# Optimization experiments

Hardware: AMD Instinct MI355X
Metric: run time of the kernel (lower is better)

The kernel has to match this reference:

```python
import jax, jax.numpy as jnp
import numpy as np

B, H, E = 1024, 2048, 1024

def _xavier(key, shape):
    # torch xavier_normal_ on [1, out, in]: std = sqrt(2/(fan_in+fan_out)) over last two dims
    fan_out, fan_in = shape[-2], shape[-1]
    std = (2.0 / (fan_in + fan_out)) ** 0.5
    return jax.random.normal(key, shape, jnp.float32) * std

def setup_inputs() -> dict:
    key = jax.random.key(0)
    ks = jax.random.split(key, 17)
    inp = {
        'x': jax.random.normal(ks[0], (B, E, 1), jnp.float32),
        'c': jax.random.normal(ks[1], (B, H, 1), jnp.float32),
        'h': jax.random.normal(ks[2], (B, H, 1), jnp.float32),
        'W_xi': _xavier(ks[3], (1, H, E)), 'W_hi': _xavier(ks[4], (1, H, H)), 'B_i': _xavier(ks[5], (1, H, 1)),
        'W_xg': _xavier(ks[6], (1, H, E)), 'W_hg': _xavier(ks[7], (1, H, H)), 'B_g': _xavier(ks[8], (1, H, 1)),
        'W_xf': _xavier(ks[9], (1, H, E)), 'W_hf': _xavier(ks[10], (1, H, H)), 'B_f': _xavier(ks[11], (1, H, 1)),
        'W_xo': _xavier(ks[12], (1, H, E)), 'W_ho': _xavier(ks[13], (1, H, H)), 'B_o': _xavier(ks[14], (1, H, 1)),
        'W_hy': _xavier(ks[15], (1, E, H)), 'B_y': _xavier(ks[16], (1, E, 1)),
    }
    return inp

def reference(x, c, h, W_xi, W_hi, B_i, W_xg, W_hg, B_g, W_xf, W_hf, B_f, W_xo, W_ho, B_o, W_hy, B_y):
    # jnp.matmul broadcasts the leading batch dim: [1,H,E] @ [B,E,1] -> [B,H,1]
    i = jax.nn.sigmoid(jnp.matmul(W_xi, x) + jnp.matmul(W_hi, h) + B_i)
    g = jnp.tanh(jnp.matmul(W_xg, x) + jnp.matmul(W_hg, h) + B_g)
    f = jax.nn.sigmoid(jnp.matmul(W_xf, x) + jnp.matmul(W_hf, h) + B_f)
    c_new = f * c + i * g
    o = jax.nn.sigmoid(jnp.matmul(W_xo, x) + jnp.matmul(W_ho, h) + B_o)
    h_new = o * c_new  # NOTE: source uses o*c (no tanh), faithful to original
    y = jnp.tanh(jnp.matmul(W_hy, h_new) + B_y)
    return (y, c_new, h_new)
```

## Files before the change

kernel.cpp:

```cpp
#include <hip/hip_runtime.h>

#define B_SZ 1024
#define H_SZ 2048
#define E_SZ 1024

typedef float  f32x4 __attribute__((ext_vector_type(4)));
typedef short  s16x8 __attribute__((ext_vector_type(8)));

__device__ __forceinline__ unsigned short f2bf(float f) {
    unsigned u = __float_as_uint(f);
    u = u + 0x7fffu + ((u >> 16) & 1u);
    return (unsigned short)(u >> 16);
}
__device__ __forceinline__ float bf2f(unsigned short s) {
    return __uint_as_float(((unsigned)s) << 16);
}
__device__ __forceinline__ float sigm(float v) {
    return 1.0f / (1.0f + __expf(-v));
}

struct SwArgs {
    const float*    src[11];
    unsigned short* dst[11];
    int             log2K[11];
    int             nthr[11];
};

__global__ __launch_bounds__(256) void swcast_kernel(SwArgs a) {
    const int arr = blockIdx.y;
    const int t = blockIdx.x * 256 + threadIdx.x;
    if (t >= a.nthr[arr]) return;
    const int lg   = a.log2K[arr];
    const int lane = t & 63;
    const int u    = t >> 6;
    const int hj   = u & 7;
    const int v    = u >> 3;
    const int k32m = (1 << (lg - 5)) - 1;
    const int ks   = v & k32m;
    const int nt   = v >> (lg - 5);
    const int row  = (nt << 7) + ((hj >> 2) << 6) + ((hj & 3) << 4) + (lane & 15);
    const int k    = (ks << 5) + ((lane >> 4) << 3);
    const float* s = a.src[arr] + ((size_t)row << lg) + k;
    float4 v0 = *(const float4*)s;
    float4 v1 = *(const float4*)(s + 4);
    s16x8 o;
    o[0] = (short)f2bf(v0.x); o[1] = (short)f2bf(v0.y);
    o[2] = (short)f2bf(v0.z); o[3] = (short)f2bf(v0.w);
    o[4] = (short)f2bf(v1.x); o[5] = (short)f2bf(v1.y);
    o[6] = (short)f2bf(v1.z); o[7] = (short)f2bf(v1.w);
    *(s16x8*)(a.dst[arr] + (size_t)t * 8) = o;
}

#define LDF(dst, base, ks)                                                  \
    _Pragma("unroll") for (int _i = 0; _i < 4; ++_i)                        \
        dst[_i] = *(const s16x8*)((base) + (ks) * 4096 + _i * 512);

#define MF(aa, bb)                                                          \
    _Pragma("unroll") for (int _i = 0; _i < 4; ++_i)                        \
    _Pragma("unroll") for (int _j = 0; _j < 4; ++_j)                        \
        acc[_i][_j] = __builtin_amdgcn_mfma_f32_16x16x32_bf16(              \
            aa[_i], bb[_j], acc[_i][_j], 0, 0, 0);

__global__ __launch_bounds__(256) void gates_kernel(
    const unsigned short* __restrict__ Xsw,
    const unsigned short* __restrict__ Hsw,
    const unsigned short* __restrict__ Wxsw,
    const unsigned short* __restrict__ Whsw,
    const float* __restrict__ bi, const float* __restrict__ bg,
    const float* __restrict__ bff, const float* __restrict__ bo,
    unsigned short* __restrict__ Z)
{
    const int t   = threadIdx.x;
    const int b   = blockIdx.x;
    const int xcd = b & 7;
    const int i_  = b >> 3;
    const int nt  = xcd * 8 + (i_ >> 3);
    const int mt  = i_ & 7;
    const int q   = nt >> 4;
    const int n0t = nt & 15;
    const int lane = t & 63, w = t >> 6;
    const int hm = w >> 1, hn = w & 1;

    const unsigned short* ax = Xsw + (size_t)(mt * 256 + hm * 4) * 512 + lane * 8;
    const unsigned short* bx = Wxsw + (size_t)q * H_SZ * E_SZ
                             + (size_t)(n0t * 256 + hn * 4) * 512 + lane * 8;
    const unsigned short* ah = Hsw + (size_t)(mt * 512 + hm * 4) * 512 + lane * 8;
    const unsigned short* bh = Whsw + (size_t)q * H_SZ * H_SZ
                             + (size_t)(n0t * 512 + hn * 4) * 512 + lane * 8;

    f32x4 acc[4][4] = {};
    s16x8 a0[4], b0[4], a1[4], b1[4];

    LDF(a0, ax, 0); LDF(b0, bx, 0);
    for (int ks = 0; ks < 30; ks += 2) {
        LDF(a1, ax, ks + 1); LDF(b1, bx, ks + 1);
        MF(a0, b0);
        LDF(a0, ax, ks + 2); LDF(b0, bx, ks + 2);
        MF(a1, b1);
    }
    LDF(a1, ax, 31); LDF(b1, bx, 31);
    MF(a0, b0);
    LDF(a0, ah, 0); LDF(b0, bh, 0);
    MF(a1, b1);
    for (int ks = 0; ks < 62; ks += 2) {
        LDF(a1, ah, ks + 1); LDF(b1, bh, ks + 1);
        MF(a0, b0);
        LDF(a0, ah, ks + 2); LDF(b0, bh, ks + 2);
        MF(a1, b1);
    }
    LDF(a1, ah, 63); LDF(b1, bh, 63);
    MF(a0, b0);
    MF(a1, b1);

    const float* bias = (q == 0) ? bi : (q == 1) ? bg : (q == 2) ? bff : bo;
    const int m0 = mt * 128, n0 = n0t * 128;
    const int wr = hm << 6, wc = hn << 6;
    const int lr = lane & 15, rq = (lane >> 4) << 2;
    unsigned short* Zq = Z + (size_t)q * B_SZ * H_SZ;
#pragma unroll
    for (int i = 0; i < 4; ++i) {
#pragma unroll
        for (int j = 0; j < 4; ++j) {
            const int n = n0 + wc + j * 16 + lr;
            const float bv = bias[n];
#pragma unroll
            for (int r = 0; r < 4; ++r) {
                const int m = m0 + wr + i * 16 + rq + r;
                const float v = acc[i][j][r] + bv;
                const float a = (q == 1) ? tanhf(v) : sigm(v);
                Zq[(size_t)m * H_SZ + n] = f2bf(a);
            }
        }
    }
}

__global__ __launch_bounds__(256) void cell_kernel(
    const unsigned short* __restrict__ Z, const float* __restrict__ c,
    float* __restrict__ c_out, float* __restrict__ h_out,
    unsigned short* __restrict__ Hnsw)
{
    const size_t BH = (size_t)B_SZ * H_SZ;
    const int t8 = blockIdx.x * 256 + threadIdx.x;
    const size_t base = (size_t)t8 * 8;

    s16x8 iu = *(const s16x8*)(Z + base);
    s16x8 gu = *(const s16x8*)(Z + BH + base);
    s16x8 fu = *(const s16x8*)(Z + 2 * BH + base);
    s16x8 ou = *(const s16x8*)(Z + 3 * BH + base);
    float4 c0 = *(const float4*)(c + base);
    float4 c1 = *(const float4*)(c + base + 4);
    const float cv[8] = {c0.x, c0.y, c0.z, c0.w, c1.x, c1.y, c1.z, c1.w};

    float cn[8], hn[8];
#pragma unroll
    for (int e = 0; e < 8; ++e) {
        cn[e] = bf2f((unsigned short)fu[e]) * cv[e]
              + bf2f((unsigned short)iu[e]) * bf2f((unsigned short)gu[e]);
        hn[e] = bf2f((unsigned short)ou[e]) * cn[e];
    }
    *(float4*)(c_out + base)     = make_float4(cn[0], cn[1], cn[2], cn[3]);
    *(float4*)(c_out + base + 4) = make_float4(cn[4], cn[5], cn[6], cn[7]);
    *(float4*)(h_out + base)     = make_float4(hn[0], hn[1], hn[2], hn[3]);
    *(float4*)(h_out + base + 4) = make_float4(hn[4], hn[5], hn[6], hn[7]);

    const int m  = (int)(base >> 11);
    const int hk = (int)(base & 2047);
    const int mt = m >> 7, half = (m >> 6) & 1, ii = (m >> 4) & 3, lr = m & 15;
    const int ks = hk >> 5, kq3 = (hk >> 3) & 3;
    const int lane2 = (kq3 << 4) | lr;
    const size_t toff = ((((size_t)mt * 64 + ks) * 8 + half * 4 + ii) * 64 + lane2) * 8;
    s16x8 hb;
#pragma unroll
    for (int e = 0; e < 8; ++e) hb[e] = (short)f2bf(hn[e]);
    *(s16x8*)(Hnsw + toff) = hb;
}

__global__ __launch_bounds__(256) void y_split_kernel(
    const unsigned short* __restrict__ Hnsw,
    const unsigned short* __restrict__ Whysw,
    float* __restrict__ part)
{
    const int t   = threadIdx.x;
    const int b   = blockIdx.x;
    const int xcd = b & 7;
    const int i_  = b >> 3;
    const int ns  = xcd * 4 + (i_ >> 3);
    const int mt  = i_ & 7;
    const int n0t = ns >> 2;
    const int s   = ns & 3;
    const int lane = t & 63, w = t >> 6;
    const int hm = w >> 1, hn = w & 1;

    const unsigned short* ay = Hnsw
        + (size_t)((mt * 64 + s * 16) * 8 + hm * 4) * 512 + lane * 8;
    const unsigned short* by = Whysw
        + (size_t)((n0t * 64 + s * 16) * 8 + hn * 4) * 512 + lane * 8;

    f32x4 acc[4][4] = {};
    s16x8 a0[4], b0[4], a1[4], b1[4];
    LDF(a0, ay, 0); LDF(b0, by, 0);
    for (int ks = 0; ks < 14; ks += 2) {
        LDF(a1, ay, ks + 1); LDF(b1, by, ks + 1);
        MF(a0, b0);
        LDF(a0, ay, ks + 2); LDF(b0, by, ks + 2);
        MF(a1, b1);
    }
    LDF(a1, ay, 15); LDF(b1, by, 15);
    MF(a0, b0);
    MF(a1, b1);

    const int m0 = mt * 128, n0 = n0t * 128;
    const int wr = hm << 6, wc = hn << 6;
    const int lr = lane & 15, rq = (lane >> 4) << 2;
    float* P = part + (size_t)s * B_SZ * E_SZ;
#pragma unroll
    for (int i = 0; i < 4; ++i) {
#pragma unroll
        for (int j = 0; j < 4; ++j) {
            const int n = n0 + wc + j * 16 + lr;
#pragma unroll
            for (int r = 0; r < 4; ++r) {
                const int m = m0 + wr + i * 16 + rq + r;
                P[(size_t)m * E_SZ + n] = acc[i][j][r];
            }
        }
    }
}

__global__ __launch_bounds__(256) void y_reduce_kernel(
    const float* __restrict__ part, const float* __restrict__ by,
    float* __restrict__ yout)
{
    const size_t BE = (size_t)B_SZ * E_SZ;
    const int idx = (blockIdx.x * 256 + threadIdx.x) * 4;
    float4 a = *(const float4*)(part + idx);
    float4 b2 = *(const float4*)(part + BE + idx);
    float4 c2 = *(const float4*)(part + 2 * BE + idx);
    float4 d2 = *(const float4*)(part + 3 * BE + idx);
    const int col = idx & (E_SZ - 1);
    float4 bv = *(const float4*)(by + col);
    float4 o;
    o.x = tanhf(a.x + b2.x + c2.x + d2.x + bv.x);
    o.y = tanhf(a.y + b2.y + c2.y + d2.y + bv.y);
    o.z = tanhf(a.z + b2.z + c2.z + d2.z + bv.z);
    o.w = tanhf(a.w + b2.w + c2.w + d2.w + bv.w);
    *(float4*)(yout + idx) = o;
}

extern "C" void kernel_launch(void* const* d_in, const int* in_sizes, int n_in,
                              void* d_out, int out_size, void* d_ws, size_t ws_size,
                              hipStream_t stream) {
    const float* x   = (const float*)d_in[0];
    const float* c   = (const float*)d_in[1];
    const float* h   = (const float*)d_in[2];
    const float* Wxi = (const float*)d_in[3];
    const float* Whi = (const float*)d_in[4];
    const float* Bi  = (const float*)d_in[5];
    const float* Wxg = (const float*)d_in[6];
    const float* Whg = (const float*)d_in[7];
    const float* Bg  = (const float*)d_in[8];
    const float* Wxf = (const float*)d_in[9];
    const float* Whf = (const float*)d_in[10];
    const float* Bf  = (const float*)d_in[11];
    const float* Wxo = (const float*)d_in[12];
    const float* Who = (const float*)d_in[13];
    const float* Bo  = (const float*)d_in[14];
    const float* Why = (const float*)d_in[15];
    const float* By  = (const float*)d_in[16];

    const size_t BE = (size_t)B_SZ * E_SZ, BH = (size_t)B_SZ * H_SZ;
    const size_t HE = (size_t)H_SZ * E_SZ, HH = (size_t)H_SZ * H_SZ;
    const size_t EH = (size_t)E_SZ * H_SZ;

    unsigned short* ws    = (unsigned short*)d_ws;
    unsigned short* Xsw   = ws;
    unsigned short* Hsw   = Xsw + BE;
    unsigned short* Wxsw  = Hsw + BH;
    unsigned short* Whsw  = Wxsw + 4 * HE;
    unsigned short* Whysw = Whsw + 4 * HH;
    unsigned short* Z     = Whysw + EH;
    unsigned short* Hnsw  = Z + 4 * BH;

    SwArgs sa;
    sa.src[0]  = x;   sa.dst[0]  = Xsw;          sa.log2K[0]  = 10; sa.nthr[0]  = (int)(BE / 8);
    sa.src[1]  = h;   sa.dst[1]  = Hsw;          sa.log2K[1]  = 11; sa.nthr[1]  = (int)(BH / 8);
    sa.src[2]  = Wxi; sa.dst[2]  = Wxsw;         sa.log2K[2]  = 10; sa.nthr[2]  = (int)(HE / 8);
    sa.src[3]  = Wxg; sa.dst[3]  = Wxsw + HE;    sa.log2K[3]  = 10; sa.nthr[3]  = (int)(HE / 8);
    sa.src[4]  = Wxf; sa.dst[4]  = Wxsw + 2*HE;  sa.log2K[4]  = 10; sa.nthr[4]  = (int)(HE / 8);
    sa.src[5]  = Wxo; sa.dst[5]  = Wxsw + 3*HE;  sa.log2K[5]  = 10; sa.nthr[5]  = (int)(HE / 8);
    sa.src[6]  = Whi; sa.dst[6]  = Whsw;         sa.log2K[6]  = 11; sa.nthr[6]  = (int)(HH / 8);
    sa.src[7]  = Whg; sa.dst[7]  = Whsw + HH;    sa.log2K[7]  = 11; sa.nthr[7]  = (int)(HH / 8);
    sa.src[8]  = Whf; sa.dst[8]  = Whsw + 2*HH;  sa.log2K[8]  = 11; sa.nthr[8]  = (int)(HH / 8);
    sa.src[9]  = Who; sa.dst[9]  = Whsw + 3*HH;  sa.log2K[9]  = 11; sa.nthr[9]  = (int)(HH / 8);
    sa.src[10] = Why; sa.dst[10] = Whysw;        sa.log2K[10] = 11; sa.nthr[10] = (int)(EH / 8);

    hipLaunchKernelGGL(swcast_kernel, dim3(2048, 11), dim3(256), 0, stream, sa);
    hipLaunchKernelGGL(gates_kernel, dim3(512), dim3(256), 0, stream,
                       Xsw, Hsw, Wxsw, Whsw, Bi, Bg, Bf, Bo, Z);

    float* y_out = (float*)d_out;
    float* c_out = y_out + BE;
    float* h_out = c_out + BH;
    hipLaunchKernelGGL(cell_kernel, dim3((unsigned)(BH / 2048)), dim3(256), 0, stream,
                       Z, c, c_out, h_out, Hnsw);

    float* ypart = (float*)Z;
    hipLaunchKernelGGL(y_split_kernel, dim3(256), dim3(256), 0, stream,
                       Hnsw, Whysw, ypart);
    hipLaunchKernelGGL(y_reduce_kernel, dim3((unsigned)(BE / 1024)), dim3(256), 0, stream,
                       ypart, By, y_out);
}
```

Measured before the change: 281.5 us.

## Fuse fp32-to-bf16 weight conversion into GEMM B-operand loads, drop weight pre-cast

```diff
diff --git a/kernel.cpp b/kernel.cpp
--- a/kernel.cpp
+++ b/kernel.cpp
@@ -20,13 +20,13 @@
 }
 
 struct SwArgs {
-    const float*    src[11];
-    unsigned short* dst[11];
-    int             log2K[11];
-    int             nthr[11];
+    const float*    src[2];
+    unsigned short* dst[2];
+    int             log2K[2];
+    int             nthr[2];
 };
 
-__global__ __launch_bounds__(256) void swcast_kernel(SwArgs a) {
+__global__ __launch_bounds__(256) void prep_kernel(SwArgs a) {
     const int arr = blockIdx.y;
     const int t = blockIdx.x * 256 + threadIdx.x;
     if (t >= a.nthr[arr]) return;
@@ -55,6 +55,27 @@
     _Pragma("unroll") for (int _i = 0; _i < 4; ++_i)                        \
         dst[_i] = *(const s16x8*)((base) + (ks) * 4096 + _i * 512);
 
+#define LDBR(raw, bp, ks, Kc)                                               \
+    _Pragma("unroll") for (int _j = 0; _j < 4; ++_j) {                      \
+        const float* _p = (bp) + (size_t)(ks) * 32 + (size_t)_j * 16 * (Kc);\
+        raw[2 * _j]     = *(const float4*)_p;                               \
+        raw[2 * _j + 1] = *(const float4*)(_p + 4);                         \
+    }
+
+#define PACKB(dst, raw)                                                     \
+    _Pragma("unroll") for (int _j = 0; _j < 4; ++_j) {                      \
+        uint4 _pk;                                                          \
+        _pk.x = __builtin_amdgcn_perm(__float_as_uint(raw[2*_j].y),         \
+                    __float_as_uint(raw[2*_j].x), 0x07060302u);             \
+        _pk.y = __builtin_amdgcn_perm(__float_as_uint(raw[2*_j].w),         \
+                    __float_as_uint(raw[2*_j].z), 0x07060302u);             \
+        _pk.z = __builtin_amdgcn_perm(__float_as_uint(raw[2*_j+1].y),       \
+                    __float_as_uint(raw[2*_j+1].x), 0x07060302u);           \
+        _pk.w = __builtin_amdgcn_perm(__float_as_uint(raw[2*_j+1].w),       \
+                    __float_as_uint(raw[2*_j+1].z), 0x07060302u);           \
+        dst[_j] = __builtin_bit_cast(s16x8, _pk);                           \
+    }
+
 #define MF(aa, bb)                                                          \
     _Pragma("unroll") for (int _i = 0; _i < 4; ++_i)                        \
     _Pragma("unroll") for (int _j = 0; _j < 4; ++_j)                        \
@@ -64,8 +85,10 @@
 __global__ __launch_bounds__(256) void gates_kernel(
     const unsigned short* __restrict__ Xsw,
     const unsigned short* __restrict__ Hsw,
-    const unsigned short* __restrict__ Wxsw,
-    const unsigned short* __restrict__ Whsw,
+    const float* __restrict__ Wxi, const float* __restrict__ Wxg,
+    const float* __restrict__ Wxf, const float* __restrict__ Wxo,
+    const float* __restrict__ Whi, const float* __restrict__ Whg,
+    const float* __restrict__ Whf, const float* __restrict__ Who,
     const float* __restrict__ bi, const float* __restrict__ bg,
     const float* __restrict__ bff, const float* __restrict__ bo,
     unsigned short* __restrict__ Z)
@@ -80,42 +103,44 @@
     const int n0t = nt & 15;
     const int lane = t & 63, w = t >> 6;
     const int hm = w >> 1, hn = w & 1;
+    const int lr = lane & 15, kq = (lane >> 4) << 3;
+    const int n0 = n0t * 128, wc = hn << 6;
 
     const unsigned short* ax = Xsw + (size_t)(mt * 256 + hm * 4) * 512 + lane * 8;
-    const unsigned short* bx = Wxsw + (size_t)q * H_SZ * E_SZ
-                             + (size_t)(n0t * 256 + hn * 4) * 512 + lane * 8;
     const unsigned short* ah = Hsw + (size_t)(mt * 512 + hm * 4) * 512 + lane * 8;
-    const unsigned short* bh = Whsw + (size_t)q * H_SZ * H_SZ
-                             + (size_t)(n0t * 512 + hn * 4) * 512 + lane * 8;
+    const float* Wxq = (q == 0) ? Wxi : (q == 1) ? Wxg : (q == 2) ? Wxf : Wxo;
+    const float* Whq = (q == 0) ? Whi : (q == 1) ? Whg : (q == 2) ? Whf : Who;
+    const float* bx = Wxq + (size_t)(n0 + wc + lr) * E_SZ + kq;
+    const float* bh = Whq + (size_t)(n0 + wc + lr) * H_SZ + kq;
 
     f32x4 acc[4][4] = {};
-    s16x8 a0[4], b0[4], a1[4], b1[4];
-
-    LDF(a0, ax, 0); LDF(b0, bx, 0);
+    s16x8 a0[4], a1[4], bfrag[4];
+    float4 r0[8], r1[8];
+
+    LDF(a0, ax, 0); LDBR(r0, bx, 0, E_SZ);
     for (int ks = 0; ks < 30; ks += 2) {
-        LDF(a1, ax, ks + 1); LDF(b1, bx, ks + 1);
-        MF(a0, b0);
-        LDF(a0, ax, ks + 2); LDF(b0, bx, ks + 2);
-        MF(a1, b1);
-    }
-    LDF(a1, ax, 31); LDF(b1, bx, 31);
-    MF(a0, b0);
-    LDF(a0, ah, 0); LDF(b0, bh, 0);
-    MF(a1, b1);
+        LDF(a1, ax, ks + 1); LDBR(r1, bx, ks + 1, E_SZ);
+        PACKB(bfrag, r0); MF(a0, bfrag);
+        LDF(a0, ax, ks + 2); LDBR(r0, bx, ks + 2, E_SZ);
+        PACKB(bfrag, r1); MF(a1, bfrag);
+    }
+    LDF(a1, ax, 31); LDBR(r1, bx, 31, E_SZ);
+    PACKB(bfrag, r0); MF(a0, bfrag);
+    LDF(a0, ah, 0); LDBR(r0, bh, 0, H_SZ);
+    PACKB(bfrag, r1); MF(a1, bfrag);
     for (int ks = 0; ks < 62; ks += 2) {
-        LDF(a1, ah, ks + 1); LDF(b1, bh, ks + 1);
-        MF(a0, b0);
-        LDF(a0, ah, ks + 2); LDF(b0, bh, ks + 2);
-        MF(a1, b1);
-    }
-    LDF(a1, ah, 63); LDF(b1, bh, 63);
-    MF(a0, b0);
-    MF(a1, b1);
+        LDF(a1, ah, ks + 1); LDBR(r1, bh, ks + 1, H_SZ);
+        PACKB(bfrag, r0); MF(a0, bfrag);
+        LDF(a0, ah, ks + 2); LDBR(r0, bh, ks + 2, H_SZ);
+        PACKB(bfrag, r1); MF(a1, bfrag);
+    }
+    LDF(a1, ah, 63); LDBR(r1, bh, 63, H_SZ);
+    PACKB(bfrag, r0); MF(a0, bfrag);
+    PACKB(bfrag, r1); MF(a1, bfrag);
 
     const float* bias = (q == 0) ? bi : (q == 1) ? bg : (q == 2) ? bff : bo;
-    const int m0 = mt * 128, n0 = n0t * 128;
-    const int wr = hm << 6, wc = hn << 6;
-    const int lr = lane & 15, rq = (lane >> 4) << 2;
+    const int m0 = mt * 128;
+    const int wr = hm << 6, rq = (lane >> 4) << 2;
     unsigned short* Zq = Z + (size_t)q * B_SZ * H_SZ;
 #pragma unroll
     for (int i = 0; i < 4; ++i) {
@@ -177,7 +202,7 @@
 
 __global__ __launch_bounds__(256) void y_split_kernel(
     const unsigned short* __restrict__ Hnsw,
-    const unsigned short* __restrict__ Whysw,
+    const float* __restrict__ Wy,
     float* __restrict__ part)
 {
     const int t   = threadIdx.x;
@@ -190,28 +215,29 @@
     const int s   = ns & 3;
     const int lane = t & 63, w = t >> 6;
     const int hm = w >> 1, hn = w & 1;
+    const int lr = lane & 15, kq = (lane >> 4) << 3;
+    const int n0 = n0t * 128, wc = hn << 6;
 
     const unsigned short* ay = Hnsw
         + (size_t)((mt * 64 + s * 16) * 8 + hm * 4) * 512 + lane * 8;
-    const unsigned short* by = Whysw
-        + (size_t)((n0t * 64 + s * 16) * 8 + hn * 4) * 512 + lane * 8;
+    const float* bp = Wy + (size_t)(n0 + wc + lr) * H_SZ + s * 512 + kq;
 
     f32x4 acc[4][4] = {};
-    s16x8 a0[4], b0[4], a1[4], b1[4];
-    LDF(a0, ay, 0); LDF(b0, by, 0);
+    s16x8 a0[4], a1[4], bfrag[4];
+    float4 r0[8], r1[8];
+    LDF(a0, ay, 0); LDBR(r0, bp, 0, H_SZ);
     for (int ks = 0; ks < 14; ks += 2) {
-        LDF(a1, ay, ks + 1); LDF(b1, by, ks + 1);
-        MF(a0, b0);
-        LDF(a0, ay, ks + 2); LDF(b0, by, ks + 2);
-        MF(a1, b1);
-    }
-    LDF(a1, ay, 15); LDF(b1, by, 15);
-    MF(a0, b0);
-    MF(a1, b1);
-
-    const int m0 = mt * 128, n0 = n0t * 128;
-    const int wr = hm << 6, wc = hn << 6;
-    const int lr = lane & 15, rq = (lane >> 4) << 2;
+        LDF(a1, ay, ks + 1); LDBR(r1, bp, ks + 1, H_SZ);
+        PACKB(bfrag, r0); MF(a0, bfrag);
+        LDF(a0, ay, ks + 2); LDBR(r0, bp, ks + 2, H_SZ);
+        PACKB(bfrag, r1); MF(a1, bfrag);
+    }
+    LDF(a1, ay, 15); LDBR(r1, bp, 15, H_SZ);
+    PACKB(bfrag, r0); MF(a0, bfrag);
+    PACKB(bfrag, r1); MF(a1, bfrag);
+
+    const int m0 = mt * 128;
+    const int wr = hm << 6, rq = (lane >> 4) << 2;
     float* P = part + (size_t)s * B_SZ * E_SZ;
 #pragma unroll
     for (int i = 0; i < 4; ++i) {
@@ -269,34 +295,21 @@
     const float* By  = (const float*)d_in[16];
 
     const size_t BE = (size_t)B_SZ * E_SZ, BH = (size_t)B_SZ * H_SZ;
-    const size_t HE = (size_t)H_SZ * E_SZ, HH = (size_t)H_SZ * H_SZ;
-    const size_t EH = (size_t)E_SZ * H_SZ;
-
-    unsigned short* ws    = (unsigned short*)d_ws;
-    unsigned short* Xsw   = ws;
-    unsigned short* Hsw   = Xsw + BE;
-    unsigned short* Wxsw  = Hsw + BH;
-    unsigned short* Whsw  = Wxsw + 4 * HE;
-    unsigned short* Whysw = Whsw + 4 * HH;
-    unsigned short* Z     = Whysw + EH;
-    unsigned short* Hnsw  = Z + 4 * BH;
+
+    unsigned short* ws   = (unsigned short*)d_ws;
+    unsigned short* Xsw  = ws;
+    unsigned short* Hsw  = Xsw + BE;
+    unsigned short* Z    = Hsw + BH;
+    unsigned short* Hnsw = Z + 4 * BH;
 
     SwArgs sa;
-    sa.src[0]  = x;   sa.dst[0]  = Xsw;          sa.log2K[0]  = 10; sa.nthr[0]  = (int)(BE / 8);
-    sa.src[1]  = h;   sa.dst[1]  = Hsw;          sa.log2K[1]  = 11; sa.nthr[1]  = (int)(BH / 8);
-    sa.src[2]  = Wxi; sa.dst[2]  = Wxsw;         sa.log2K[2]  = 10; sa.nthr[2]  = (int)(HE / 8);
-    sa.src[3]  = Wxg; sa.dst[3]  = Wxsw + HE;    sa.log2K[3]  = 10; sa.nthr[3]  = (int)(HE / 8);
-    sa.src[4]  = Wxf; sa.dst[4]  = Wxsw + 2*HE;  sa.log2K[4]  = 10; sa.nthr[4]  = (int)(HE / 8);
-    sa.src[5]  = Wxo; sa.dst[5]  = Wxsw + 3*HE;  sa.log2K[5]  = 10; sa.nthr[5]  = (int)(HE / 8);
-    sa.src[6]  = Whi; sa.dst[6]  = Whsw;         sa.log2K[6]  = 11; sa.nthr[6]  = (int)(HH / 8);
-    sa.src[7]  = Whg; sa.dst[7]  = Whsw + HH;    sa.log2K[7]  = 11; sa.nthr[7]  = (int)(HH / 8);
-    sa.src[8]  = Whf; sa.dst[8]  = Whsw + 2*HH;  sa.log2K[8]  = 11; sa.nthr[8]  = (int)(HH / 8);
-    sa.src[9]  = Who; sa.dst[9]  = Whsw + 3*HH;  sa.log2K[9]  = 11; sa.nthr[9]  = (int)(HH / 8);
-    sa.src[10] = Why; sa.dst[10] = Whysw;        sa.log2K[10] = 11; sa.nthr[10] = (int)(EH / 8);
-
-    hipLaunchKernelGGL(swcast_kernel, dim3(2048, 11), dim3(256), 0, stream, sa);
+    sa.src[0] = x; sa.dst[0] = Xsw; sa.log2K[0] = 10; sa.nthr[0] = (int)(BE / 8);
+    sa.src[1] = h; sa.dst[1] = Hsw; sa.log2K[1] = 11; sa.nthr[1] = (int)(BH / 8);
+
+    hipLaunchKernelGGL(prep_kernel, dim3(1024, 2), dim3(256), 0, stream, sa);
     hipLaunchKernelGGL(gates_kernel, dim3(512), dim3(256), 0, stream,
-                       Xsw, Hsw, Wxsw, Whsw, Bi, Bg, Bf, Bo, Z);
+                       Xsw, Hsw, Wxi, Wxg, Wxf, Wxo, Whi, Whg, Whf, Who,
+                       Bi, Bg, Bf, Bo, Z);
 
     float* y_out = (float*)d_out;
     float* c_out = y_out + BE;
@@ -306,7 +319,7 @@
 
     float* ypart = (float*)Z;
     hipLaunchKernelGGL(y_split_kernel, dim3(256), dim3(256), 0, stream,
-                       Hnsw, Whysw, ypart);
+                       Hnsw, Why, ypart);
     hipLaunchKernelGGL(y_reduce_kernel, dim3((unsigned)(BE / 1024)), dim3(256), 0, stream,
                        ypart, By, y_out);
 }
```

New measurement: 401.9 us. 42.8% more time.
